# Kernel tuning notes

Hardware: AMD Instinct MI355X
Metric: run time of the kernel (lower is better)

Reference implementation:

```python
import jax, jax.numpy as jnp
import numpy as np

B, CIN, T = 64, 64, 4096
F, K = 128, 64


def setup_inputs() -> dict:
    key = jax.random.key(0)
    k1, k2, k3, k4, k5 = jax.random.split(key, 5)
    x = jax.random.normal(k1, (B, CIN, T), dtype=jnp.float32)
    conv_weights = jax.random.normal(k2, (F, K), dtype=jnp.float32) * 0.2
    spat_weights = jax.random.normal(k3, (F, CIN), dtype=jnp.float32) * 0.2
    weight = jax.random.normal(k4, (F,), dtype=jnp.float32)
    bias = jax.random.normal(k5, (F,), dtype=jnp.float32)
    return {"x": x, "conv_weights": conv_weights, "spat_weights": spat_weights,
            "weight": weight, "bias": bias}


def reference(x, conv_weights, spat_weights, weight, bias):
    n_filters, ksize = conv_weights.shape
    n_in = spat_weights.shape[1]
    # rank-1 merged kernel: [F, Cin, K]
    merged = conv_weights[:, None, :] * spat_weights[:, :, None]
    # valid conv1d: x [B,Cin,T] -> conved [B,F,T-K+1]
    conved = jax.lax.conv_general_dilated(
        x, merged, window_strides=(1,), padding='VALID',
        dimension_numbers=('NCH', 'OIH', 'NCH'))
    # per-filter weight norm
    norm_w = jnp.sqrt(jnp.sum(merged * merged, axis=(1, 2)))  # [F]
    # input norm: sliding-window sum of x^2 over channels and window
    sq = jnp.sum(x * x, axis=1, keepdims=True)  # [B,1,T]
    ones_k = jnp.ones((1, 1, ksize), dtype=x.dtype)
    slide = jax.lax.conv_general_dilated(
        sq, ones_k, window_strides=(1,), padding='VALID',
        dimension_numbers=('NCH', 'OIH', 'NCH'))[:, 0, :]  # [B,Tout]
    norm_inputs = jnp.sqrt(slide)
    scale = np.sqrt(n_in * ksize).astype(np.float32)
    cos_sims = conved / (norm_w[None, :, None] * norm_inputs[:, None, :]) * scale
    mean_cos = jnp.mean(jnp.abs(cos_sims), axis=2)  # [B,F]
    out_per_wave = mean_cos * weight[None, :] + bias[None, :]
    return jnp.sum(out_per_wave, axis=1)  # [B]
```

## Files before the change

### kernel.cpp

```cpp
#include <hip/hip_runtime.h>
#include <hip/hip_bf16.h>
#include <cstdint>
#include <cstddef>

#define BB   64
#define CINN 64
#define TS   4096
#define FF   128
#define KS   64
#define TOUT (TS - KS + 1)

#define TSEG 256
#define XROW 320
#define SXW  324
#define YW   336
#define YWW  (YW / 2)

typedef __attribute__((ext_vector_type(8))) short short8;
typedef __attribute__((ext_vector_type(4))) float f32x4;
union FragU { unsigned int u[4]; short8 v; uint4 q4; };

static __device__ __forceinline__ unsigned int f2bf_u(float f) {
    __hip_bfloat16 h = __float2bfloat16(f);
    return (unsigned int)*reinterpret_cast<unsigned short*>(&h);
}

__global__ void k_band(const float* __restrict__ cw, const float* __restrict__ sw,
                       const float* __restrict__ weight,
                       uint4* __restrict__ bandB, float* __restrict__ wnf,
                       uint4* __restrict__ swF) {
    const int f = blockIdx.x, l = threadIdx.x;
    const int n = l & 15, q = l >> 4;
    for (int s = 0; s < 3; ++s) {
        FragU o;
#pragma unroll
        for (int i = 0; i < 4; ++i) {
            int i0 = 32 * s + 8 * q + 2 * i - n;
            int i1 = i0 + 1;
            float a = (i0 >= 0 && i0 < KS) ? cw[(size_t)f * KS + i0] : 0.f;
            float c = (i1 >= 0 && i1 < KS) ? cw[(size_t)f * KS + i1] : 0.f;
            o.u[i] = f2bf_u(a) | (f2bf_u(c) << 16);
        }
        bandB[((size_t)f * 3 + s) * 64 + l] = o.q4;
    }
    if ((f & 15) == 0) {
        const int ft = f >> 4;
        for (int s = 0; s < 2; ++s) {
            FragU o;
#pragma unroll
            for (int i = 0; i < 4; ++i) {
                const float* sr = sw + (size_t)(16 * ft + n) * CINN + 32 * s + 8 * q + 2 * i;
                o.u[i] = f2bf_u(sr[0]) | (f2bf_u(sr[1]) << 16);
            }
            swF[((size_t)ft * 2 + s) * 64 + l] = o.q4;
        }
    }
    float a = sw[(size_t)f * CINN + l], c = cw[(size_t)f * KS + l];
    float v = a * a, u = c * c;
    for (int off = 32; off > 0; off >>= 1) {
        v += __shfl_down(v, off, 64);
        u += __shfl_down(u, off, 64);
    }
    if (l == 0) wnf[f] = weight[f] * rsqrtf(v * u) * (64.0f / (float)TOUT);
}

__global__ __launch_bounds__(1024, 4) void k_fused(
    const float* __restrict__ x, const uint4* __restrict__ swF,
    const uint4* __restrict__ bandB, const float* __restrict__ wnf,
    const float* __restrict__ bias, float* __restrict__ out)
{
    __shared__ unsigned int xT[34 * SXW];
    __shared__ uint4 swFl[1024];
    __shared__ unsigned int yL[FF * YWW];
    __shared__ float wred[16];

    const int tid = threadIdx.x;
    const int w = tid >> 6, l = tid & 63;
    const int m = l & 15, q = l >> 4;
    const int b = blockIdx.y;
    const int t0 = blockIdx.x * TSEG;

    swFl[tid] = swF[tid];

    {
        const float* xb = x + (size_t)b * CINN * TS;
        float* sqp = (float*)yL;
        float4 s4a = {0.f, 0.f, 0.f, 0.f}, s4b = {0.f, 0.f, 0.f, 0.f};
#pragma unroll
        for (int r = 0; r < 2; ++r) {
            const int cp = w + 16 * r;
            const float* x0 = xb + (size_t)(2 * cp) * TS;
            {
                int p = t0 + 4 * l; if (p > TS - 4) p = TS - 4;
                float4 v0 = *(const float4*)(x0 + p);
                float4 v1 = *(const float4*)(x0 + TS + p);
                s4a.x += v0.x * v0.x + v1.x * v1.x;
                s4a.y += v0.y * v0.y + v1.y * v1.y;
                s4a.z += v0.z * v0.z + v1.z * v1.z;
                s4a.w += v0.w * v0.w + v1.w * v1.w;
                FragU o;
                o.u[0] = f2bf_u(v0.x) | (f2bf_u(v1.x) << 16);
                o.u[1] = f2bf_u(v0.y) | (f2bf_u(v1.y) << 16);
                o.u[2] = f2bf_u(v0.z) | (f2bf_u(v1.z) << 16);
                o.u[3] = f2bf_u(v0.w) | (f2bf_u(v1.w) << 16);
                *(uint4*)&xT[cp * SXW + 4 * l] = o.q4;
            }
            if (l < 16) {
                int p = t0 + 256 + 4 * l; if (p > TS - 4) p = TS - 4;
                float4 v0 = *(const float4*)(x0 + p);
                float4 v1 = *(const float4*)(x0 + TS + p);
                s4b.x += v0.x * v0.x + v1.x * v1.x;
                s4b.y += v0.y * v0.y + v1.y * v1.y;
                s4b.z += v0.z * v0.z + v1.z * v1.z;
                s4b.w += v0.w * v0.w + v1.w * v1.w;
                FragU o;
                o.u[0] = f2bf_u(v0.x) | (f2bf_u(v1.x) << 16);
                o.u[1] = f2bf_u(v0.y) | (f2bf_u(v1.y) << 16);
                o.u[2] = f2bf_u(v0.z) | (f2bf_u(v1.z) << 16);
                o.u[3] = f2bf_u(v0.w) | (f2bf_u(v1.w) << 16);
                *(uint4*)&xT[cp * SXW + 256 + 4 * l] = o.q4;
            }
        }
        *(float4*)(sqp + w * XROW + 4 * l) = s4a;
        if (l < 16) *(float4*)(sqp + w * XROW + 256 + 4 * l) = s4b;
    }
    __syncthreads();

    if (tid < XROW) {
        const float* sqp = (const float*)yL;
        float s = 0.f;
#pragma unroll
        for (int i = 0; i < 16; ++i) s += sqp[i * XROW + tid];
        xT[32 * SXW + tid] = __float_as_uint(s);
    }
    __syncthreads();

    if (w == 15 && l < 32) {
        const int base = 8 * l;
        float s = 0.f, hd[8], tl[8];
#pragma unroll
        for (int k = 0; k < 64; ++k) {
            float v = __uint_as_float(xT[32 * SXW + base + k]);
            if (k < 8) hd[k] = v;
            s += v;
        }
#pragma unroll
        for (int j = 0; j < 8; ++j) tl[j] = __uint_as_float(xT[32 * SXW + base + 64 + j]);
#pragma unroll
        for (int j = 0; j < 8; ++j) {
            int tpos = t0 + base + j;
            float rv = (tpos < TOUT) ? rsqrtf(s) : 0.f;
            xT[33 * SXW + base + j] = __float_as_uint(rv);
            s += tl[j] - hd[j];
        }
    }

    {
        const int quad = w & 1;
        for (int tt = (w >> 1); tt < 20; tt += 8) {
            FragU b0, b1;
#pragma unroll
            for (int i = 0; i < 4; ++i) {
                b0.u[i] = xT[(4 * q + i) * SXW + 16 * tt + m];
                b1.u[i] = xT[(16 + 4 * q + i) * SXW + 16 * tt + m];
            }
#pragma unroll 1
            for (int fi = 0; fi < 4; ++fi) {
                FragU s0, s1;
                s0.q4 = swFl[((4 * quad + fi) * 2 + 0) * 64 + l];
                s1.q4 = swFl[((4 * quad + fi) * 2 + 1) * 64 + l];
                f32x4 d = {0.f, 0.f, 0.f, 0.f};
                d = __builtin_amdgcn_mfma_f32_16x16x32_bf16(b0.v, s0.v, d, 0, 0, 0);
                d = __builtin_amdgcn_mfma_f32_16x16x32_bf16(b1.v, s1.v, d, 0, 0, 0);
                const int f = 16 * (4 * quad + fi) + m;
                uint2 o;
                o.x = f2bf_u(d[0]) | (f2bf_u(d[1]) << 16);
                o.y = f2bf_u(d[2]) | (f2bf_u(d[3]) << 16);
                *(uint2*)(yL + f * YWW + 8 * tt + 2 * q) = o;
            }
        }
        yL[(tid >> 3) * YWW + 160 + (tid & 7)] = 0u;
    }
    __syncthreads();

    float acc = 0.f;
    {
        float rr[4];
#pragma unroll
        for (int r = 0; r < 4; ++r) {
            int t = 64 * q + 16 * r + m;
            rr[r] = __uint_as_float(xT[33 * SXW + t]);
        }
        const int f0t = 8 * w;
        uint4 pb0, pb1, pb2;
        {
            const uint4* bb = bandB + (size_t)f0t * 3 * 64;
            pb0 = bb[l]; pb1 = bb[64 + l]; pb2 = bb[128 + l];
        }
#pragma unroll 2
        for (int fi = 0; fi < 8; ++fi) {
            const int f = f0t + fi;
            FragU B0, B1, B2;
            B0.q4 = pb0; B1.q4 = pb1; B2.q4 = pb2;
            if (fi < 7) {
                const uint4* bb = bandB + (size_t)(f + 1) * 3 * 64;
                pb0 = bb[l]; pb1 = bb[64 + l]; pb2 = bb[128 + l];
            }
            const int abase = f * YWW + 8 * m + 4 * q;
            FragU a0, a1, a2;
            a0.q4 = *(const uint4*)(yL + abase);
            a1.q4 = *(const uint4*)(yL + abase + 16);
            a2.q4 = *(const uint4*)(yL + abase + 32);
            f32x4 d = {0.f, 0.f, 0.f, 0.f};
            d = __builtin_amdgcn_mfma_f32_16x16x32_bf16(a0.v, B0.v, d, 0, 0, 0);
            d = __builtin_amdgcn_mfma_f32_16x16x32_bf16(a1.v, B1.v, d, 0, 0, 0);
            d = __builtin_amdgcn_mfma_f32_16x16x32_bf16(a2.v, B2.v, d, 0, 0, 0);
            float facc = 0.f;
#pragma unroll
            for (int r = 0; r < 4; ++r) facc += fabsf(d[r]) * rr[r];
            acc += wnf[f] * facc;
        }
    }

    for (int off = 32; off > 0; off >>= 1) acc += __shfl_down(acc, off, 64);
    if (l == 0) wred[w] = acc;
    __syncthreads();
    if (tid == 0) {
        float s = 0.f;
#pragma unroll
        for (int i = 0; i < 16; ++i) s += wred[i];
        atomicAdd(out + b, s);
    }
    if (blockIdx.x == 0 && tid < FF) {
        float v = bias[tid];
        for (int off = 32; off > 0; off >>= 1) v += __shfl_down(v, off, 64);
        if ((tid & 63) == 0) atomicAdd(out + b, v);
    }
}

__global__ __launch_bounds__(256) void k_naive(
    const float* __restrict__ x, const float* __restrict__ cw,
    const float* __restrict__ sw, const float* __restrict__ weight,
    const float* __restrict__ bias, float* __restrict__ out)
{
    __shared__ float yl[TS];
    __shared__ float ql[TS];
    __shared__ float wred[4];
    const int f = blockIdx.x, b = blockIdx.y, tid = threadIdx.x;
    for (int t = tid; t < TS; t += 256) {
        float a = 0.f, s = 0.f;
        for (int c = 0; c < CINN; ++c) {
            float v = x[((size_t)b * CINN + c) * TS + t];
            a += sw[(size_t)f * CINN + c] * v;
            s += v * v;
        }
        yl[t] = a; ql[t] = s;
    }
    __syncthreads();
    float acc = 0.f;
    for (int t = tid; t < TOUT; t += 256) {
        float cv = 0.f, sl = 0.f;
        for (int k = 0; k < KS; ++k) { cv += cw[(size_t)f * KS + k] * yl[t + k]; sl += ql[t + k]; }
        acc += fabsf(cv) * rsqrtf(sl);
    }
    float ssw = 0.f, scw = 0.f;
    for (int c = 0; c < CINN; ++c) { float v = sw[(size_t)f * CINN + c]; ssw += v * v; }
    for (int k = 0; k < KS; ++k)   { float v = cw[(size_t)f * KS + k];  scw += v * v; }
    const float wnf = weight[f] * rsqrtf(ssw * scw) * 64.0f / (float)TOUT;
    for (int off = 32; off > 0; off >>= 1) acc += __shfl_down(acc, off, 64);
    if ((tid & 63) == 0) wred[tid >> 6] = acc;
    __syncthreads();
    if (tid == 0) {
        float tot = (wred[0] + wred[1] + wred[2] + wred[3]) * wnf;
        if (f == 0) {
            float bsum = 0.f;
            for (int ff = 0; ff < FF; ++ff) bsum += bias[ff];
            tot += bsum;
        }
        atomicAdd(out + b, tot);
    }
}

extern "C" void kernel_launch(void* const* d_in, const int* in_sizes, int n_in,
                              void* d_out, int out_size, void* d_ws, size_t ws_size,
                              hipStream_t stream) {
    const float* x  = (const float*)d_in[0];
    const float* cw = (const float*)d_in[1];
    const float* sw = (const float*)d_in[2];
    const float* w  = (const float*)d_in[3];
    const float* bs = (const float*)d_in[4];
    float* out = (float*)d_out;

    hipMemsetAsync(d_out, 0, (size_t)out_size * sizeof(float), stream);

    const size_t bandBytes = (size_t)FF * 3 * 64 * 16;
    const size_t wnBytes   = (size_t)FF * sizeof(float);
    const size_t swfBytes  = (size_t)(FF / 16) * 2 * 64 * 16;

    if (bandBytes + wnBytes + swfBytes <= ws_size) {
        uint4* bandB = (uint4*)d_ws;
        float* wnf   = (float*)((char*)d_ws + bandBytes);
        uint4* swF   = (uint4*)((char*)d_ws + bandBytes + wnBytes);
        k_band <<<dim3(FF), 64, 0, stream>>>(cw, sw, w, bandB, wnf, swF);
        k_fused<<<dim3(TS / TSEG, BB), 1024, 0, stream>>>(x, swF, bandB, wnf, bs, out);
    } else {
        k_naive<<<dim3(FF, BB), 256, 0, stream>>>(x, cw, sw, w, bs, out);
    }
}
```

Baseline: 136.1 us.

## Process filters in groups of 32 to shrink LDS and raise occupancy

The intermediate per-filter buffer is shrunk from all 128 filters to a 32-filter group, and the two conv stages loop over four groups with barriers between them. The shared spatial-weight copy is dropped and fragments are read straight from global memory, while the squared-sum and inverse-norm arrays move into small separate buffers. Launch bounds now ask for 8 blocks per CU instead of 4, aiming to fit more blocks into LDS. The cost is extra __syncthreads per group, repeated global loads of weight fragments, and a tighter register budget that may cause spills.

```diff
diff --git a/kernel.cpp b/kernel.cpp
--- a/kernel.cpp
+++ b/kernel.cpp
@@ -13,8 +13,8 @@
 #define TSEG 256
 #define XROW 320
 #define SXW  324
-#define YW   336
-#define YWW  (YW / 2)
+#define YWW  168
+#define GF   32
 
 typedef __attribute__((ext_vector_type(8))) short short8;
 typedef __attribute__((ext_vector_type(4))) float f32x4;
@@ -64,14 +64,15 @@
     if (l == 0) wnf[f] = weight[f] * rsqrtf(v * u) * (64.0f / (float)TOUT);
 }
 
-__global__ __launch_bounds__(1024, 4) void k_fused(
+__global__ __launch_bounds__(1024, 8) void k_fused(
     const float* __restrict__ x, const uint4* __restrict__ swF,
     const uint4* __restrict__ bandB, const float* __restrict__ wnf,
     const float* __restrict__ bias, float* __restrict__ out)
 {
-    __shared__ unsigned int xT[34 * SXW];
-    __shared__ uint4 swFl[1024];
-    __shared__ unsigned int yL[FF * YWW];
+    __shared__ unsigned int xT[32 * SXW];
+    __shared__ unsigned int yL[GF * YWW];
+    __shared__ float sqA[XROW];
+    __shared__ float rinvA[XROW];
     __shared__ float wred[16];
 
     const int tid = threadIdx.x;
@@ -79,8 +80,6 @@
     const int m = l & 15, q = l >> 4;
     const int b = blockIdx.y;
     const int t0 = blockIdx.x * TSEG;
-
-    swFl[tid] = swF[tid];
 
     {
         const float* xb = x + (size_t)b * CINN * TS;
@@ -131,7 +130,7 @@
         float s = 0.f;
 #pragma unroll
         for (int i = 0; i < 16; ++i) s += sqp[i * XROW + tid];
-        xT[32 * SXW + tid] = __float_as_uint(s);
+        sqA[tid] = s;
     }
     __syncthreads();
 
@@ -140,86 +139,75 @@
         float s = 0.f, hd[8], tl[8];
 #pragma unroll
         for (int k = 0; k < 64; ++k) {
-            float v = __uint_as_float(xT[32 * SXW + base + k]);
+            float v = sqA[base + k];
             if (k < 8) hd[k] = v;
             s += v;
         }
 #pragma unroll
-        for (int j = 0; j < 8; ++j) tl[j] = __uint_as_float(xT[32 * SXW + base + 64 + j]);
+        for (int j = 0; j < 8; ++j) tl[j] = sqA[base + 64 + j];
 #pragma unroll
         for (int j = 0; j < 8; ++j) {
             int tpos = t0 + base + j;
-            float rv = (tpos < TOUT) ? rsqrtf(s) : 0.f;
-            xT[33 * SXW + base + j] = __float_as_uint(rv);
+            rinvA[base + j] = (tpos < TOUT) ? rsqrtf(s) : 0.f;
             s += tl[j] - hd[j];
         }
     }
 
-    {
-        const int quad = w & 1;
-        for (int tt = (w >> 1); tt < 20; tt += 8) {
-            FragU b0, b1;
-#pragma unroll
-            for (int i = 0; i < 4; ++i) {
-                b0.u[i] = xT[(4 * q + i) * SXW + 16 * tt + m];
-                b1.u[i] = xT[(16 + 4 * q + i) * SXW + 16 * tt + m];
-            }
-#pragma unroll 1
-            for (int fi = 0; fi < 4; ++fi) {
+    float acc = 0.f;
+    for (int g = 0; g < 4; ++g) {
+        {
+            const int quad = w & 1;
+            const int ft = 2 * g + quad;
+            for (int tt = (w >> 1); tt < 20; tt += 8) {
+                FragU b0, b1;
+#pragma unroll
+                for (int i = 0; i < 4; ++i) {
+                    b0.u[i] = xT[(4 * q + i) * SXW + 16 * tt + m];
+                    b1.u[i] = xT[(16 + 4 * q + i) * SXW + 16 * tt + m];
+                }
                 FragU s0, s1;
-                s0.q4 = swFl[((4 * quad + fi) * 2 + 0) * 64 + l];
-                s1.q4 = swFl[((4 * quad + fi) * 2 + 1) * 64 + l];
+                s0.q4 = swF[((size_t)ft * 2 + 0) * 64 + l];
+                s1.q4 = swF[((size_t)ft * 2 + 1) * 64 + l];
                 f32x4 d = {0.f, 0.f, 0.f, 0.f};
                 d = __builtin_amdgcn_mfma_f32_16x16x32_bf16(b0.v, s0.v, d, 0, 0, 0);
                 d = __builtin_amdgcn_mfma_f32_16x16x32_bf16(b1.v, s1.v, d, 0, 0, 0);
-                const int f = 16 * (4 * quad + fi) + m;
+                const int fl = 16 * quad + m;
                 uint2 o;
                 o.x = f2bf_u(d[0]) | (f2bf_u(d[1]) << 16);
                 o.y = f2bf_u(d[2]) | (f2bf_u(d[3]) << 16);
-                *(uint2*)(yL + f * YWW + 8 * tt + 2 * q) = o;
-            }
-        }
-        yL[(tid >> 3) * YWW + 160 + (tid & 7)] = 0u;
-    }
-    __syncthreads();
-
-    float acc = 0.f;
-    {
-        float rr[4];
-#pragma unroll
-        for (int r = 0; r < 4; ++r) {
-            int t = 64 * q + 16 * r + m;
-            rr[r] = __uint_as_float(xT[33 * SXW + t]);
-        }
-        const int f0t = 8 * w;
-        uint4 pb0, pb1, pb2;
+                *(uint2*)(yL + fl * YWW + 8 * tt + 2 * q) = o;
+            }
+            if (g == 0 && tid < 256) yL[(tid >> 3) * YWW + 160 + (tid & 7)] = 0u;
+        }
+        __syncthreads();
+
         {
-            const uint4* bb = bandB + (size_t)f0t * 3 * 64;
-            pb0 = bb[l]; pb1 = bb[64 + l]; pb2 = bb[128 + l];
-        }
-#pragma unroll 2
-        for (int fi = 0; fi < 8; ++fi) {
-            const int f = f0t + fi;
-            FragU B0, B1, B2;
-            B0.q4 = pb0; B1.q4 = pb1; B2.q4 = pb2;
-            if (fi < 7) {
-                const uint4* bb = bandB + (size_t)(f + 1) * 3 * 64;
-                pb0 = bb[l]; pb1 = bb[64 + l]; pb2 = bb[128 + l];
-            }
-            const int abase = f * YWW + 8 * m + 4 * q;
-            FragU a0, a1, a2;
-            a0.q4 = *(const uint4*)(yL + abase);
-            a1.q4 = *(const uint4*)(yL + abase + 16);
-            a2.q4 = *(const uint4*)(yL + abase + 32);
-            f32x4 d = {0.f, 0.f, 0.f, 0.f};
-            d = __builtin_amdgcn_mfma_f32_16x16x32_bf16(a0.v, B0.v, d, 0, 0, 0);
-            d = __builtin_amdgcn_mfma_f32_16x16x32_bf16(a1.v, B1.v, d, 0, 0, 0);
-            d = __builtin_amdgcn_mfma_f32_16x16x32_bf16(a2.v, B2.v, d, 0, 0, 0);
-            float facc = 0.f;
-#pragma unroll
-            for (int r = 0; r < 4; ++r) facc += fabsf(d[r]) * rr[r];
-            acc += wnf[f] * facc;
-        }
+            float rr[4];
+#pragma unroll
+            for (int r = 0; r < 4; ++r) rr[r] = rinvA[64 * q + 16 * r + m];
+#pragma unroll
+            for (int j = 0; j < 2; ++j) {
+                const int fl = 2 * w + j;
+                const int f  = GF * g + fl;
+                const uint4* bb = bandB + (size_t)f * 3 * 64;
+                FragU B0, B1, B2;
+                B0.q4 = bb[l]; B1.q4 = bb[64 + l]; B2.q4 = bb[128 + l];
+                const int abase = fl * YWW + 8 * m + 4 * q;
+                FragU a0, a1, a2;
+                a0.q4 = *(const uint4*)(yL + abase);
+                a1.q4 = *(const uint4*)(yL + abase + 16);
+                a2.q4 = *(const uint4*)(yL + abase + 32);
+                f32x4 d = {0.f, 0.f, 0.f, 0.f};
+                d = __builtin_amdgcn_mfma_f32_16x16x32_bf16(a0.v, B0.v, d, 0, 0, 0);
+                d = __builtin_amdgcn_mfma_f32_16x16x32_bf16(a1.v, B1.v, d, 0, 0, 0);
+                d = __builtin_amdgcn_mfma_f32_16x16x32_bf16(a2.v, B2.v, d, 0, 0, 0);
+                float facc = 0.f;
+#pragma unroll
+                for (int r = 0; r < 4; ++r) facc += fabsf(d[r]) * rr[r];
+                acc += wnf[f] * facc;
+            }
+        }
+        __syncthreads();
     }
 
     for (int off = 32; off > 0; off >>= 1) acc += __shfl_down(acc, off, 64);
```

After: 143.7 us. 5.6% more time.
